# Kernel tuning notes

Measured on AMD Instinct MI355X. Metric: run time of the kernel, lower is better.

Reference implementation:

```python
import jax, jax.numpy as jnp
import numpy as np

N_ATOMS = 1_000_000
N_GRAPHS = 8192
FEA_DIM = 64
HIDDEN = 32
N_HEAD = 3


def setup_inputs() -> dict:
    key = jax.random.key(0)
    k1, k2, k3, k4, k5, k6 = jax.random.split(key, 6)
    atom_feas = jax.random.normal(k1, (N_ATOMS, FEA_DIM), dtype=jnp.float32)
    atom_owner = jnp.sort(jax.random.randint(k2, (N_ATOMS,), 0, N_GRAPHS))
    s1 = 1.0 / np.sqrt(FEA_DIM)
    s2 = 1.0 / np.sqrt(HIDDEN)
    W1 = jax.random.uniform(k3, (FEA_DIM, HIDDEN), jnp.float32, -s1, s1)
    b1 = jax.random.uniform(k4, (HIDDEN,), jnp.float32, -s1, s1)
    W2 = jax.random.uniform(k5, (HIDDEN, N_HEAD), jnp.float32, -s2, s2)
    b2 = jax.random.uniform(k6, (N_HEAD,), jnp.float32, -s2, s2)
    return {"atom_feas": atom_feas, "atom_owner": atom_owner,
            "W1": W1, "b1": b1, "W2": W2, "b2": b2}


def reference(atom_feas, atom_owner, W1, b1, W2, b2):
    # key MLP: Linear -> SiLU -> Linear, producing per-atom, per-head logits [N, H]
    h = jax.nn.silu(atom_feas @ W1 + b1)
    logits = h @ W2 + b2  # [N, H]
    # per-graph (segment) softmax over atoms, independently per head
    seg_max = jax.ops.segment_max(logits, atom_owner, num_segments=N_GRAPHS)  # [G, H]
    e = jnp.exp(logits - seg_max[atom_owner])
    denom = jax.ops.segment_sum(e, atom_owner, num_segments=N_GRAPHS)  # [G, H]
    w = e / denom[atom_owner]  # [N, H]
    # attention-weighted pooling: per graph, atom_fea.T @ w -> [D, H] flattened row-major
    outer = (atom_feas[:, :, None] * w[:, None, :]).reshape(atom_feas.shape[0], FEA_DIM * N_HEAD)
    crystal_feas = jax.ops.segment_sum(outer, atom_owner, num_segments=N_GRAPHS)  # [G, D*H]
    return crystal_feas
```

## Files before the change

### kernel.cpp

```cpp
#include <hip/hip_runtime.h>
#include <math.h>
#include <stdint.h>

#define NFEA   64
#define NHEAD  3
#define K1_T   256
#define K1_TILE 256
#define GPB    4
#define LCAP   256

typedef float v2f __attribute__((ext_vector_type(2)));

__device__ __forceinline__ void wave_sync_lds() {
  asm volatile("s_waitcnt lgkmcnt(0)" ::: "memory");
}

__global__ void gar_starts(const int* __restrict__ owner, int* __restrict__ starts,
                           int n_atoms, int n_graphs)
{
  int a = blockIdx.x * blockDim.x + threadIdx.x;
  if (a >= n_atoms) return;
  int cur  = owner[a];
  int prev = (a == 0) ? -1 : owner[a - 1];
  for (int g = prev + 1; g <= cur; ++g) starts[g] = a;
  if (a == n_atoms - 1)
    for (int g = cur + 1; g <= n_graphs; ++g) starts[g] = n_atoms;
}

__global__ __launch_bounds__(K1_T, 1) void gar_mlp(
    const float* __restrict__ atom_feas,
    const float* __restrict__ W1, const float* __restrict__ b1,
    const float* __restrict__ W2, const float* __restrict__ b2,
    float4* __restrict__ logits4, int n_atoms, int n_tiles)
{
  __shared__ __align__(16) float xs[2][K1_TILE * NFEA];
  const int tid = threadIdx.x;
  const int w = tid >> 6, t = tid & 63;
  const char* __restrict__ xbytes = (const char*)atom_feas;

  auto STAGE = [&](int tile, int buf) {
    const unsigned base_row = (unsigned)tile * K1_TILE;
#pragma unroll
    for (int j = 0; j < 16; ++j) {
      const int r = ((j * 4 + w) << 2) + (t >> 4);
      unsigned grow = base_row + (unsigned)r;
      if (grow >= (unsigned)n_atoms) grow = (unsigned)n_atoms - 1;
      const unsigned src = grow * 256u + (unsigned)((((t & 15) ^ (r & 15)) << 4));
      __builtin_amdgcn_global_load_lds(
          (const __attribute__((address_space(1))) void*)(xbytes + src),
          (__attribute__((address_space(3))) void*)
              ((char*)&xs[buf][0] + ((j * 4 + w) << 10) + (t << 4)),
          16, 0, 0);
    }
  };

  int tile = blockIdx.x;
  if (tile >= n_tiles) return;
  STAGE(tile, 0);
  int buf = 0;
  const int key = (tid & 15);

  for (; tile < n_tiles; tile += gridDim.x) {
    const int nxt = tile + gridDim.x;
    if (nxt < n_tiles) {
      STAGE(nxt, buf ^ 1);
      asm volatile("s_waitcnt vmcnt(16)" ::: "memory");
    } else {
      asm volatile("s_waitcnt vmcnt(0)" ::: "memory");
    }
    asm volatile("" ::: "memory");
    __builtin_amdgcn_s_barrier();
    asm volatile("" ::: "memory");

    const float* xrow = &xs[buf][tid * 64];
    v2f h[16];
#pragma unroll
    for (int j = 0; j < 16; ++j) h[j] = ((const v2f*)b1)[j];
#pragma unroll
    for (int q = 0; q < 16; ++q) {
      float4 xq = *(const float4*)(xrow + ((q ^ key) << 2));
      float xsc[4] = {xq.x, xq.y, xq.z, xq.w};
#pragma unroll
      for (int dd = 0; dd < 4; ++dd) {
        v2f xd2 = {xsc[dd], xsc[dd]};
        const v2f* wrow = ((const v2f*)W1) + (q * 4 + dd) * 16;
#pragma unroll
        for (int jj = 0; jj < 16; ++jj)
          h[jj] = __builtin_elementwise_fma(xd2, wrow[jj], h[jj]);
      }
    }
    float l0 = b2[0], l1 = b2[1], l2 = b2[2];
#pragma unroll
    for (int jj = 0; jj < 16; ++jj) {
#pragma unroll
      for (int cc = 0; cc < 2; ++cc) {
        float hj = h[jj][cc];
        float s = hj * __builtin_amdgcn_rcpf(1.0f + __expf(-hj));
        int k = 2 * jj + cc;
        l0 = fmaf(s, W2[k * 3 + 0], l0);
        l1 = fmaf(s, W2[k * 3 + 1], l1);
        l2 = fmaf(s, W2[k * 3 + 2], l2);
      }
    }
    const int aabs = tile * K1_TILE + tid;
    if (aabs < n_atoms) logits4[aabs] = make_float4(l0, l1, l2, 0.f);

    asm volatile("" ::: "memory");
    __builtin_amdgcn_s_barrier();
    asm volatile("" ::: "memory");
    buf ^= 1;
  }
}

__global__ __launch_bounds__(GPB * 64, 8) void gar_pool(
    const float* __restrict__ atom_feas,
    const int*   __restrict__ starts,
    const float4* __restrict__ logits4,
    float* __restrict__ out, int n_graphs)
{
  __shared__ __align__(16) float4 e4[GPB][LCAP];
  const int w = threadIdx.x >> 6, t = threadIdx.x & 63;
  const int g = blockIdx.x * GPB + w;
  if (g >= n_graphs) return;
  const int s0 = starts[g];
  const int n  = starts[g + 1] - s0;
  float* __restrict__ outg = out + (size_t)g * (NFEA * NHEAD);
  if (n <= 0) {
    outg[t * 3 + 0] = 0.f; outg[t * 3 + 1] = 0.f; outg[t * 3 + 2] = 0.f;
    return;
  }

  float lr[4][3];
  float m0 = -INFINITY, m1 = -INFINITY, m2 = -INFINITY;
#pragma unroll
  for (int c = 0; c < 4; ++c) {
    if (c * 64 < n) {
      int i = c * 64 + t;
      bool act = i < n;
      float4 lv = logits4[s0 + (act ? i : 0)];
      lr[c][0] = act ? lv.x : -INFINITY;
      lr[c][1] = act ? lv.y : -INFINITY;
      lr[c][2] = act ? lv.z : -INFINITY;
      m0 = fmaxf(m0, lr[c][0]); m1 = fmaxf(m1, lr[c][1]); m2 = fmaxf(m2, lr[c][2]);
    } else {
      lr[c][0] = -INFINITY; lr[c][1] = -INFINITY; lr[c][2] = -INFINITY;
    }
  }
  for (int i = 4 * 64 + t; i < n; i += 64) {
    float4 lv = logits4[s0 + i];
    m0 = fmaxf(m0, lv.x); m1 = fmaxf(m1, lv.y); m2 = fmaxf(m2, lv.z);
  }
#pragma unroll
  for (int off = 32; off > 0; off >>= 1) {
    m0 = fmaxf(m0, __shfl_xor(m0, off));
    m1 = fmaxf(m1, __shfl_xor(m1, off));
    m2 = fmaxf(m2, __shfl_xor(m2, off));
  }

  float d0 = 0.f, d1 = 0.f, d2 = 0.f;
#pragma unroll
  for (int c = 0; c < 4; ++c) {
    if (c * 64 < n) {
      float e0 = __expf(lr[c][0] - m0);
      float e1 = __expf(lr[c][1] - m1);
      float e2 = __expf(lr[c][2] - m2);
      d0 += e0; d1 += e1; d2 += e2;
      e4[w][c * 64 + t] = make_float4(e0, e1, e2, 0.f);
    }
  }
  for (int i = 4 * 64 + t; i < n; i += 64) {
    float4 lv = logits4[s0 + i];
    d0 += __expf(lv.x - m0); d1 += __expf(lv.y - m1); d2 += __expf(lv.z - m2);
  }
#pragma unroll
  for (int off = 32; off > 0; off >>= 1) {
    d0 += __shfl_xor(d0, off);
    d1 += __shfl_xor(d1, off);
    d2 += __shfl_xor(d2, off);
  }
  wave_sync_lds();

  float a0 = 0.f, a1 = 0.f, a2 = 0.f;
  const float* __restrict__ xcol = atom_feas + (size_t)s0 * NFEA + t;
  const int nmain = n < LCAP ? n : LCAP;
#pragma unroll 4
  for (int a = 0; a < nmain; ++a) {
    float  xv = xcol[(size_t)a * NFEA];
    float4 ev = e4[w][a];
    a0 = fmaf(ev.x, xv, a0);
    a1 = fmaf(ev.y, xv, a1);
    a2 = fmaf(ev.z, xv, a2);
  }
  for (int a = LCAP; a < n; ++a) {
    float4 lv = logits4[s0 + a];
    float  xv = xcol[(size_t)a * NFEA];
    a0 = fmaf(__expf(lv.x - m0), xv, a0);
    a1 = fmaf(__expf(lv.y - m1), xv, a1);
    a2 = fmaf(__expf(lv.z - m2), xv, a2);
  }

  const float i0 = 1.f / d0, i1 = 1.f / d1, i2 = 1.f / d2;
  outg[t * 3 + 0] = a0 * i0;
  outg[t * 3 + 1] = a1 * i1;
  outg[t * 3 + 2] = a2 * i2;
}

extern "C" void kernel_launch(void* const* d_in, const int* in_sizes, int n_in,
                              void* d_out, int out_size, void* d_ws, size_t ws_size,
                              hipStream_t stream)
{
  const float* atom_feas = (const float*)d_in[0];
  const int*   owner     = (const int*)d_in[1];
  const float* W1        = (const float*)d_in[2];
  const float* b1        = (const float*)d_in[3];
  const float* W2        = (const float*)d_in[4];
  const float* b2        = (const float*)d_in[5];
  float* out = (float*)d_out;

  const int n_atoms  = in_sizes[1];
  const int n_graphs = out_size / (NFEA * NHEAD);

  int* starts = (int*)d_ws;
  const size_t log_off = (((size_t)(n_graphs + 1) * sizeof(int)) + 255) & ~(size_t)255;
  float4* logits4 = (float4*)((char*)d_ws + log_off);

  const int n_tiles = (n_atoms + K1_TILE - 1) / K1_TILE;
  const int k1_grid = n_tiles < 256 ? n_tiles : 256;

  hipLaunchKernelGGL(gar_starts, dim3((n_atoms + 255) / 256), dim3(256), 0, stream,
                     owner, starts, n_atoms, n_graphs);
  hipLaunchKernelGGL(gar_mlp, dim3(k1_grid), dim3(K1_T), 0, stream,
                     atom_feas, W1, b1, W2, b2, logits4, n_atoms, n_tiles);
  hipLaunchKernelGGL(gar_pool, dim3((n_graphs + GPB - 1) / GPB), dim3(GPB * 64), 0, stream,
                     atom_feas, starts, logits4, out, n_graphs);
}
```

Measured before the change: 501.1 us.

## Replace LDS-staged persistent MLP kernel with direct per-thread row loads

The MLP kernel drops its persistent grid with double-buffered global_load_lds staging into shared memory. Each thread now loads its own 256-byte atom row straight into 16 float4 registers, one block per 256 atoms, with launch bounds allowing 4 blocks per CU. This removes the LDS traffic, the barriers and the swizzle logic, leaving latency hiding to occupancy. The cost is uncoalesced strided row loads across lanes, since each lane reads a different 256-byte row, and higher register pressure.

Measured after the change: 418.3 us. 16.5% less time.

```diff
diff --git a/kernel.cpp b/kernel.cpp
--- a/kernel.cpp
+++ b/kernel.cpp
@@ -4,8 +4,6 @@
 
 #define NFEA   64
 #define NHEAD  3
-#define K1_T   256
-#define K1_TILE 256
 #define GPB    4
 #define LCAP   256
 
@@ -27,89 +25,51 @@
     for (int g = cur + 1; g <= n_graphs; ++g) starts[g] = n_atoms;
 }
 
-__global__ __launch_bounds__(K1_T, 1) void gar_mlp(
+__global__ __launch_bounds__(256, 4) void gar_mlp(
     const float* __restrict__ atom_feas,
     const float* __restrict__ W1, const float* __restrict__ b1,
     const float* __restrict__ W2, const float* __restrict__ b2,
-    float4* __restrict__ logits4, int n_atoms, int n_tiles)
+    float4* __restrict__ logits4, int n_atoms)
 {
-  __shared__ __align__(16) float xs[2][K1_TILE * NFEA];
-  const int tid = threadIdx.x;
-  const int w = tid >> 6, t = tid & 63;
-  const char* __restrict__ xbytes = (const char*)atom_feas;
+  const int a = blockIdx.x * 256 + threadIdx.x;
+  if (a >= n_atoms) return;
+  const float4* __restrict__ xrow = (const float4*)(atom_feas + (size_t)a * NFEA);
 
-  auto STAGE = [&](int tile, int buf) {
-    const unsigned base_row = (unsigned)tile * K1_TILE;
+  float4 xr[16];
 #pragma unroll
-    for (int j = 0; j < 16; ++j) {
-      const int r = ((j * 4 + w) << 2) + (t >> 4);
-      unsigned grow = base_row + (unsigned)r;
-      if (grow >= (unsigned)n_atoms) grow = (unsigned)n_atoms - 1;
-      const unsigned src = grow * 256u + (unsigned)((((t & 15) ^ (r & 15)) << 4));
-      __builtin_amdgcn_global_load_lds(
-          (const __attribute__((address_space(1))) void*)(xbytes + src),
-          (__attribute__((address_space(3))) void*)
-              ((char*)&xs[buf][0] + ((j * 4 + w) << 10) + (t << 4)),
-          16, 0, 0);
+  for (int q = 0; q < 16; ++q) xr[q] = xrow[q];
+
+  v2f h[16];
+#pragma unroll
+  for (int j = 0; j < 16; ++j) h[j] = ((const v2f*)b1)[j];
+
+#pragma unroll
+  for (int q = 0; q < 16; ++q) {
+    float xs[4] = {xr[q].x, xr[q].y, xr[q].z, xr[q].w};
+#pragma unroll
+    for (int dd = 0; dd < 4; ++dd) {
+      v2f xd2 = {xs[dd], xs[dd]};
+      const v2f* wrow = ((const v2f*)W1) + (q * 4 + dd) * 16;
+#pragma unroll
+      for (int jj = 0; jj < 16; ++jj)
+        h[jj] = __builtin_elementwise_fma(xd2, wrow[jj], h[jj]);
     }
-  };
+  }
 
-  int tile = blockIdx.x;
-  if (tile >= n_tiles) return;
-  STAGE(tile, 0);
-  int buf = 0;
-  const int key = (tid & 15);
-
-  for (; tile < n_tiles; tile += gridDim.x) {
-    const int nxt = tile + gridDim.x;
-    if (nxt < n_tiles) {
-      STAGE(nxt, buf ^ 1);
-      asm volatile("s_waitcnt vmcnt(16)" ::: "memory");
-    } else {
-      asm volatile("s_waitcnt vmcnt(0)" ::: "memory");
+  float l0 = b2[0], l1 = b2[1], l2 = b2[2];
+#pragma unroll
+  for (int jj = 0; jj < 16; ++jj) {
+#pragma unroll
+    for (int cc = 0; cc < 2; ++cc) {
+      float hj = h[jj][cc];
+      float s = hj * __builtin_amdgcn_rcpf(1.0f + __expf(-hj));
+      int k = 2 * jj + cc;
+      l0 = fmaf(s, W2[k * 3 + 0], l0);
+      l1 = fmaf(s, W2[k * 3 + 1], l1);
+      l2 = fmaf(s, W2[k * 3 + 2], l2);
     }
-    asm volatile("" ::: "memory");
-    __builtin_amdgcn_s_barrier();
-    asm volatile("" ::: "memory");
-
-    const float* xrow = &xs[buf][tid * 64];
-    v2f h[16];
-#pragma unroll
-    for (int j = 0; j < 16; ++j) h[j] = ((const v2f*)b1)[j];
-#pragma unroll
-    for (int q = 0; q < 16; ++q) {
-      float4 xq = *(const float4*)(xrow + ((q ^ key) << 2));
-      float xsc[4] = {xq.x, xq.y, xq.z, xq.w};
-#pragma unroll
-      for (int dd = 0; dd < 4; ++dd) {
-        v2f xd2 = {xsc[dd], xsc[dd]};
-        const v2f* wrow = ((const v2f*)W1) + (q * 4 + dd) * 16;
-#pragma unroll
-        for (int jj = 0; jj < 16; ++jj)
-          h[jj] = __builtin_elementwise_fma(xd2, wrow[jj], h[jj]);
-      }
-    }
-    float l0 = b2[0], l1 = b2[1], l2 = b2[2];
-#pragma unroll
-    for (int jj = 0; jj < 16; ++jj) {
-#pragma unroll
-      for (int cc = 0; cc < 2; ++cc) {
-        float hj = h[jj][cc];
-        float s = hj * __builtin_amdgcn_rcpf(1.0f + __expf(-hj));
-        int k = 2 * jj + cc;
-        l0 = fmaf(s, W2[k * 3 + 0], l0);
-        l1 = fmaf(s, W2[k * 3 + 1], l1);
-        l2 = fmaf(s, W2[k * 3 + 2], l2);
-      }
-    }
-    const int aabs = tile * K1_TILE + tid;
-    if (aabs < n_atoms) logits4[aabs] = make_float4(l0, l1, l2, 0.f);
-
-    asm volatile("" ::: "memory");
-    __builtin_amdgcn_s_barrier();
-    asm volatile("" ::: "memory");
-    buf ^= 1;
   }
+  logits4[a] = make_float4(l0, l1, l2, 0.f);
 }
 
 __global__ __launch_bounds__(GPB * 64, 8) void gar_pool(
@@ -224,13 +184,10 @@
   const size_t log_off = (((size_t)(n_graphs + 1) * sizeof(int)) + 255) & ~(size_t)255;
   float4* logits4 = (float4*)((char*)d_ws + log_off);
 
-  const int n_tiles = (n_atoms + K1_TILE - 1) / K1_TILE;
-  const int k1_grid = n_tiles < 256 ? n_tiles : 256;
-
   hipLaunchKernelGGL(gar_starts, dim3((n_atoms + 255) / 256), dim3(256), 0, stream,
                      owner, starts, n_atoms, n_graphs);
-  hipLaunchKernelGGL(gar_mlp, dim3(k1_grid), dim3(K1_T), 0, stream,
-                     atom_feas, W1, b1, W2, b2, logits4, n_atoms, n_tiles);
+  hipLaunchKernelGGL(gar_mlp, dim3((n_atoms + 255) / 256), dim3(256), 0, stream,
+                     atom_feas, W1, b1, W2, b2, logits4, n_atoms);
   hipLaunchKernelGGL(gar_pool, dim3((n_graphs + GPB - 1) / GPB), dim3(GPB * 64), 0, stream,
                      atom_feas, starts, logits4, out, n_graphs);
 }
```
